# Performance work log

Hardware: AMD Instinct MI355X
Metric: run time of the kernel (lower is better)

## Reference

```python
import jax, jax.numpy as jnp
import numpy as np

B, N, DIN, DE, NH, DK = 4, 256, 128, 64, 8, 16


def setup_inputs() -> dict:
    key = jax.random.key(0)
    ks = jax.random.split(key, 8)
    s = 0.05
    return {
        "h": jax.random.normal(ks[0], (B, N, DIN), jnp.float32),
        "e": jax.random.normal(ks[1], (B, N, N, DE), jnp.float32),
        "mask": jnp.ones((B, N), jnp.float32),
        "WQ": jax.random.normal(ks[2], (DIN, NH * DK), jnp.float32) * s,
        "WK": jax.random.normal(ks[3], (DIN, NH * DK), jnp.float32) * s,
        "WV": jax.random.normal(ks[4], (DIN, NH * DK), jnp.float32) * s,
        "WE": jax.random.normal(ks[5], (DE, NH * DK), jnp.float32) * s,
        "WE2": jax.random.normal(ks[6], (DE, NH * DK), jnp.float32) * s,
    }


def reference(h, e, mask, WQ, WK, WV, WE, WE2):
    b, n, _ = h.shape
    Q = (h @ WQ).reshape(b, n, NH, DK)
    K = (h @ WK).reshape(b, n, NH, DK) * (float(DK) ** -0.5)
    V = (h @ WV).reshape(b, n, NH, DK)
    E = (e @ WE).reshape(b, n, n, NH, DK)
    E2 = (e @ WE2).reshape(b, n, n, NH, DK)
    # edge-augmented scores: (b, i, j, h, k)
    scores = jnp.einsum('bihk,bjhk->bijh', Q, K)[..., None] + E2
    scores = jnp.exp(jnp.clip(scores, -5.0, 5.0))
    attn_mask = mask[:, :, None, None, None] * mask[:, None, :, None, None]
    scores = scores * attn_mask
    softmax_denom = jnp.clip(scores.sum(axis=2), 1e-6, None)  # (b,i,h,k)
    scores = scores * attn_mask  # attn_dropout p=0.0 -> identity
    out = jnp.einsum('bijhk,bjhk->bihk', scores, V)
    out = out + (scores * E).sum(axis=2)
    out = out / softmax_denom
    return out.reshape(b, n, NH * DK)
```

## Files before the change

kernel.cpp:

```cpp
#include <hip/hip_runtime.h>

#define BB   4
#define NN   256
#define DIN  128
#define DE   64
#define NH   8
#define DK   16
#define CC   128

typedef __attribute__((ext_vector_type(8))) short short8;
typedef __attribute__((ext_vector_type(4))) float f32x4;

__device__ __forceinline__ unsigned short f2bfu(float f) {
    union { float f; unsigned int i; } v; v.f = f;
    unsigned int x = v.i;
    x += 0x7FFFu + ((x >> 16) & 1u);
    return (unsigned short)(x >> 16);
}

__global__ __launch_bounds__(256) void wprep_kernel(
    const float* __restrict__ WE, const float* __restrict__ WE2,
    unsigned short* __restrict__ wfrag)
{
    const int tid  = blockIdx.x * 256 + threadIdx.x;
    const int m    = tid >> 10;
    const int g    = (tid >> 7) & 7;
    const int ks   = (tid >> 6) & 1;
    const int lane = tid & 63;
    const int q4 = lane >> 4, l15 = lane & 15;
    const float* W = m ? WE2 : WE;
    union { uint4 u; unsigned short s[8]; } pk;
    #pragma unroll
    for (int ii = 0; ii < 8; ++ii) {
        const int d = ks * 32 + q4 * 8 + ii;
        pk.s[ii] = f2bfu(W[d * CC + g * 16 + l15]);
    }
    ((uint4*)wfrag)[tid] = pk.u;
}

__global__ __launch_bounds__(256) void qkv_kernel(
    const float* __restrict__ h, const float* __restrict__ WQ,
    const float* __restrict__ WK, const float* __restrict__ WV,
    float* __restrict__ Qw, float* __restrict__ Kw, float* __restrict__ Vw)
{
    __shared__ float hsh[4 * DIN];
    __shared__ float psum[4 * 1536];
    const int t  = threadIdx.x;
    const int r0 = blockIdx.x * 4;

    hsh[t]       = h[(size_t)r0 * DIN + t];
    hsh[256 + t] = h[(size_t)r0 * DIN + 256 + t];
    __syncthreads();

    const int cp  = t & 63;
    const int qtr = t >> 6;
    float aq[4][2], ak[4][2], av[4][2];
    #pragma unroll
    for (int r = 0; r < 4; ++r) {
        aq[r][0]=aq[r][1]=ak[r][0]=ak[r][1]=av[r][0]=av[r][1]=0.f;
    }
    #pragma unroll 4
    for (int dd = 0; dd < 32; ++dd) {
        const int d = qtr * 32 + dd;
        const float2 fq = ((const float2*)WQ)[d * 64 + cp];
        const float2 fk = ((const float2*)WK)[d * 64 + cp];
        const float2 fv = ((const float2*)WV)[d * 64 + cp];
        #pragma unroll
        for (int r = 0; r < 4; ++r) {
            const float hd = hsh[r * DIN + d];
            aq[r][0] = fmaf(hd, fq.x, aq[r][0]); aq[r][1] = fmaf(hd, fq.y, aq[r][1]);
            ak[r][0] = fmaf(hd, fk.x, ak[r][0]); ak[r][1] = fmaf(hd, fk.y, ak[r][1]);
            av[r][0] = fmaf(hd, fv.x, av[r][0]); av[r][1] = fmaf(hd, fv.y, av[r][1]);
        }
    }
    float* pq = psum + qtr * 1536;
    #pragma unroll
    for (int r = 0; r < 4; ++r) {
        pq[r*384       + 2*cp] = aq[r][0]; pq[r*384       + 2*cp+1] = aq[r][1];
        pq[r*384 + 128 + 2*cp] = ak[r][0]; pq[r*384 + 128 + 2*cp+1] = ak[r][1];
        pq[r*384 + 256 + 2*cp] = av[r][0]; pq[r*384 + 256 + 2*cp+1] = av[r][1];
    }
    __syncthreads();
    #pragma unroll
    for (int k = 0; k < 6; ++k) {
        const int o = k * 256 + t;
        float v = psum[o] + psum[1536 + o] + psum[3072 + o] + psum[4608 + o];
        const int r   = o / 384;
        const int mc  = o - r * 384;
        const int mat = mc >> 7;
        const int c   = mc & 127;
        const size_t idx = (size_t)(r0 + r) * CC + c;
        if      (mat == 0) Qw[idx] = v;
        else if (mat == 1) Kw[idx] = v * 0.25f;
        else               Vw[idx] = v;
    }
}

__global__ __launch_bounds__(256, 3) void attn_kernel(
    const float* __restrict__ e, const float* __restrict__ maskp,
    const unsigned short* __restrict__ wfrag,
    const float* __restrict__ Qw, const float* __restrict__ Kw,
    const float* __restrict__ Vw, float* __restrict__ out)
{
    __shared__ __align__(16) unsigned short esh[NN * DE];
    __shared__ float qk_sh[NN * 9];
    __shared__ float msk_sh[NN];
    __shared__ float qrow_sh[CC];

    const int row  = blockIdx.x;
    const int b    = row >> 8, i = row & 255;
    const int t    = threadIdx.x;
    const int wave = t >> 6, lane = t & 63;
    const int q4   = lane >> 4;
    const int l15  = lane & 15;

    {
        const float4* src = (const float4*)(e + (size_t)row * NN * DE);
        uint4* dst = (uint4*)esh;
        #pragma unroll
        for (int r = 0; r < 8; ++r) {
            const int cidx = r * 256 + t;
            const int j = cidx >> 3, ch = cidx & 7;
            const float4 f0 = src[2 * cidx];
            const float4 f1 = src[2 * cidx + 1];
            union { uint4 u; unsigned short s[8]; } pk;
            pk.s[0]=f2bfu(f0.x); pk.s[1]=f2bfu(f0.y); pk.s[2]=f2bfu(f0.z); pk.s[3]=f2bfu(f0.w);
            pk.s[4]=f2bfu(f1.x); pk.s[5]=f2bfu(f1.y); pk.s[6]=f2bfu(f1.z); pk.s[7]=f2bfu(f1.w);
            dst[j * 8 + (ch ^ (j & 7))] = pk.u;
        }
    }
    if (t < CC) qrow_sh[t] = Qw[(size_t)row * CC + t];
    msk_sh[t] = maskp[b * NN + t];

    short8 bfrag[2][2][2];
    {
        const uint4* wf = (const uint4*)wfrag;
        #pragma unroll
        for (int m = 0; m < 2; ++m)
        #pragma unroll
        for (int ct = 0; ct < 2; ++ct) {
            const int g = wave * 2 + ct;
            #pragma unroll
            for (int ks = 0; ks < 2; ++ks) {
                union { uint4 u; short8 s8; } cv;
                cv.u = wf[((m * 8 + g) * 2 + ks) * 64 + lane];
                bfrag[m][ct][ks] = cv.s8;
            }
        }
    }
    __syncthreads();

    {
        const float4* kr = (const float4*)(Kw + (size_t)(b * NN + t) * CC);
        #pragma unroll
        for (int hh = 0; hh < NH; ++hh) {
            float s = 0.f;
            #pragma unroll
            for (int p = 0; p < 4; ++p) {
                const float4 kv = kr[hh * 4 + p];
                const int qb = hh * 16 + p * 4;
                s += kv.x * qrow_sh[qb]     + kv.y * qrow_sh[qb + 1]
                   + kv.z * qrow_sh[qb + 2] + kv.w * qrow_sh[qb + 3];
            }
            qk_sh[t * 9 + hh] = s;
        }
    }
    __syncthreads();

    const float mi = msk_sh[i];
    float acc[2] = {0.f, 0.f}, dnm[2] = {0.f, 0.f};
    const short8* ep = (const short8*)esh;

    #pragma unroll 2
    for (int s = 0; s < 16; ++s) {
        const int ja = s * 16 + l15;
        const short8 a0 = ep[ja * 8 + ((q4    ) ^ (ja & 7))];
        const short8 a1 = ep[ja * 8 + ((q4 + 4) ^ (ja & 7))];
        #pragma unroll
        for (int ct = 0; ct < 2; ++ct) {
            const int g = wave * 2 + ct;
            f32x4 s2 = {0.f,0.f,0.f,0.f}, eE = {0.f,0.f,0.f,0.f};
            s2 = __builtin_amdgcn_mfma_f32_16x16x32_bf16(a0, bfrag[1][ct][0], s2, 0,0,0);
            s2 = __builtin_amdgcn_mfma_f32_16x16x32_bf16(a1, bfrag[1][ct][1], s2, 0,0,0);
            eE = __builtin_amdgcn_mfma_f32_16x16x32_bf16(a0, bfrag[0][ct][0], eE, 0,0,0);
            eE = __builtin_amdgcn_mfma_f32_16x16x32_bf16(a1, bfrag[0][ct][1], eE, 0,0,0);
            const float* vrow = Vw + (size_t)(b*NN + s*16 + q4*4) * CC + g*16 + l15;
            #pragma unroll
            for (int r = 0; r < 4; ++r) {
                const int jr = s * 16 + q4 * 4 + r;
                float sc = qk_sh[jr * 9 + g] + s2[r];
                sc = fminf(5.f, fmaxf(-5.f, sc));
                const float p  = __expf(sc);
                const float mm = mi * msk_sh[jr];
                const float s1 = p * mm;
                dnm[ct] += s1;
                const float vv = vrow[r * CC];
                acc[ct] = fmaf(s1 * mm, vv + eE[r], acc[ct]);
            }
        }
    }

    #pragma unroll
    for (int ct = 0; ct < 2; ++ct) {
        float a = acc[ct], d = dnm[ct];
        a += __shfl_xor(a, 16); a += __shfl_xor(a, 32);
        d += __shfl_xor(d, 16); d += __shfl_xor(d, 32);
        acc[ct] = a; dnm[ct] = d;
    }
    if (lane < 32) {
        const int ct = lane >> 4;
        out[(size_t)row * CC + wave * 32 + lane] = acc[ct] / fmaxf(dnm[ct], 1e-6f);
    }
}

extern "C" void kernel_launch(void* const* d_in, const int* in_sizes, int n_in,
                              void* d_out, int out_size, void* d_ws, size_t ws_size,
                              hipStream_t stream)
{
    const float* h    = (const float*)d_in[0];
    const float* e    = (const float*)d_in[1];
    const float* mask = (const float*)d_in[2];
    const float* WQ   = (const float*)d_in[3];
    const float* WK   = (const float*)d_in[4];
    const float* WV   = (const float*)d_in[5];
    const float* WE   = (const float*)d_in[6];
    const float* WE2  = (const float*)d_in[7];

    unsigned short* wfrag = (unsigned short*)d_ws;
    float* Qw = (float*)((char*)d_ws + 32768);
    float* Kw = Qw + BB * NN * CC;
    float* Vw = Kw + BB * NN * CC;

    wprep_kernel<<<8,   256, 0, stream>>>(WE, WE2, wfrag);
    qkv_kernel <<<256,  256, 0, stream>>>(h, WQ, WK, WV, Qw, Kw, Vw);
    attn_kernel<<<BB*NN, 256, 0, stream>>>(e, mask, wfrag, Qw, Kw, Vw,
                                           (float*)d_out);
}
```

Baseline: 139.9 us.

## Stream edge tiles through triple-buffered LDS and merge prep kernels

The attention kernel no longer stages the whole 256x64 edge row in LDS up front. It now loads 32-row tiles into registers one step ahead, converts them to bf16, and writes them into a 3-slot LDS ring, so global loads overlap with MFMA work. This shrinks LDS use and raises the occupancy hint from 3 to 4 blocks per CU. The weight-fragment prep and the QKV projection are also merged into a single launch to save one kernel launch. In exchange, the loop now has a barrier every tile and holds more registers for the prefetch.

```diff
diff --git a/kernel.cpp b/kernel.cpp
--- a/kernel.cpp
+++ b/kernel.cpp
@@ -18,36 +18,36 @@
     return (unsigned short)(x >> 16);
 }
 
-__global__ __launch_bounds__(256) void wprep_kernel(
-    const float* __restrict__ WE, const float* __restrict__ WE2,
-    unsigned short* __restrict__ wfrag)
-{
-    const int tid  = blockIdx.x * 256 + threadIdx.x;
-    const int m    = tid >> 10;
-    const int g    = (tid >> 7) & 7;
-    const int ks   = (tid >> 6) & 1;
-    const int lane = tid & 63;
-    const int q4 = lane >> 4, l15 = lane & 15;
-    const float* W = m ? WE2 : WE;
-    union { uint4 u; unsigned short s[8]; } pk;
-    #pragma unroll
-    for (int ii = 0; ii < 8; ++ii) {
-        const int d = ks * 32 + q4 * 8 + ii;
-        pk.s[ii] = f2bfu(W[d * CC + g * 16 + l15]);
-    }
-    ((uint4*)wfrag)[tid] = pk.u;
-}
-
-__global__ __launch_bounds__(256) void qkv_kernel(
+__global__ __launch_bounds__(256) void prep_kernel(
     const float* __restrict__ h, const float* __restrict__ WQ,
     const float* __restrict__ WK, const float* __restrict__ WV,
-    float* __restrict__ Qw, float* __restrict__ Kw, float* __restrict__ Vw)
+    const float* __restrict__ WE, const float* __restrict__ WE2,
+    float* __restrict__ Qw, float* __restrict__ Kw, float* __restrict__ Vw,
+    unsigned short* __restrict__ wfrag)
 {
     __shared__ float hsh[4 * DIN];
     __shared__ float psum[4 * 1536];
-    const int t  = threadIdx.x;
+    const int t = threadIdx.x;
+
+    if (blockIdx.x >= 256) {
+        const int tid  = (blockIdx.x - 256) * 256 + t;
+        const int m    = tid >> 10;
+        const int g    = (tid >> 7) & 7;
+        const int ks   = (tid >> 6) & 1;
+        const int lane = tid & 63;
+        const int q4 = lane >> 4, l15 = lane & 15;
+        const float* W = m ? WE2 : WE;
+        union { uint4 u; unsigned short s[8]; } pk;
+        #pragma unroll
+        for (int ii = 0; ii < 8; ++ii) {
+            const int d = ks * 32 + q4 * 8 + ii;
+            pk.s[ii] = f2bfu(W[d * CC + g * 16 + l15]);
+        }
+        ((uint4*)wfrag)[tid] = pk.u;
+        return;
+    }
+
     const int r0 = blockIdx.x * 4;
-
     hsh[t]       = h[(size_t)r0 * DIN + t];
     hsh[256 + t] = h[(size_t)r0 * DIN + 256 + t];
     __syncthreads();
@@ -96,13 +96,13 @@
     }
 }
 
-__global__ __launch_bounds__(256, 3) void attn_kernel(
+__global__ __launch_bounds__(256, 4) void attn_kernel(
     const float* __restrict__ e, const float* __restrict__ maskp,
     const unsigned short* __restrict__ wfrag,
     const float* __restrict__ Qw, const float* __restrict__ Kw,
     const float* __restrict__ Vw, float* __restrict__ out)
 {
-    __shared__ __align__(16) unsigned short esh[NN * DE];
+    __shared__ __align__(16) unsigned short esh[3][32 * DE];
     __shared__ float qk_sh[NN * 9];
     __shared__ float msk_sh[NN];
     __shared__ float qrow_sh[CC];
@@ -114,21 +114,16 @@
     const int q4   = lane >> 4;
     const int l15  = lane & 15;
 
-    {
-        const float4* src = (const float4*)(e + (size_t)row * NN * DE);
-        uint4* dst = (uint4*)esh;
-        #pragma unroll
-        for (int r = 0; r < 8; ++r) {
-            const int cidx = r * 256 + t;
-            const int j = cidx >> 3, ch = cidx & 7;
-            const float4 f0 = src[2 * cidx];
-            const float4 f1 = src[2 * cidx + 1];
-            union { uint4 u; unsigned short s[8]; } pk;
-            pk.s[0]=f2bfu(f0.x); pk.s[1]=f2bfu(f0.y); pk.s[2]=f2bfu(f0.z); pk.s[3]=f2bfu(f0.w);
-            pk.s[4]=f2bfu(f1.x); pk.s[5]=f2bfu(f1.y); pk.s[6]=f2bfu(f1.z); pk.s[7]=f2bfu(f1.w);
-            dst[j * 8 + (ch ^ (j & 7))] = pk.u;
-        }
-    }
+    const int sj_ = t >> 3;
+    const int sch = t & 7;
+    const float4* esrc = (const float4*)(e + (size_t)row * NN * DE)
+                         + (size_t)sj_ * 16 + sch * 2;
+    uint4* eshv = (uint4*)esh;
+
+    float4 pf[2][2];
+    pf[0][0] = esrc[0];       pf[0][1] = esrc[1];
+    pf[1][0] = esrc[512];     pf[1][1] = esrc[512 + 1];
+
     if (t < CC) qrow_sh[t] = Qw[(size_t)row * CC + t];
     msk_sh[t] = maskp[b * NN + t];
 
@@ -165,40 +160,61 @@
             qk_sh[t * 9 + hh] = s;
         }
     }
+
+#define STORE_TILE(BUF, F0, F1) {                                              \
+        union { uint4 u; unsigned short s[8]; } pk;                            \
+        pk.s[0]=f2bfu((F0).x); pk.s[1]=f2bfu((F0).y);                          \
+        pk.s[2]=f2bfu((F0).z); pk.s[3]=f2bfu((F0).w);                          \
+        pk.s[4]=f2bfu((F1).x); pk.s[5]=f2bfu((F1).y);                          \
+        pk.s[6]=f2bfu((F1).z); pk.s[7]=f2bfu((F1).w);                          \
+        eshv[(BUF)*256 + sj_*8 + (sch ^ (sj_ & 7))] = pk.u; }
+
+    STORE_TILE(0, pf[0][0], pf[0][1]);
     __syncthreads();
 
     const float mi = msk_sh[i];
     float acc[2] = {0.f, 0.f}, dnm[2] = {0.f, 0.f};
-    const short8* ep = (const short8*)esh;
-
-    #pragma unroll 2
-    for (int s = 0; s < 16; ++s) {
-        const int ja = s * 16 + l15;
-        const short8 a0 = ep[ja * 8 + ((q4    ) ^ (ja & 7))];
-        const short8 a1 = ep[ja * 8 + ((q4 + 4) ^ (ja & 7))];
-        #pragma unroll
-        for (int ct = 0; ct < 2; ++ct) {
-            const int g = wave * 2 + ct;
-            f32x4 s2 = {0.f,0.f,0.f,0.f}, eE = {0.f,0.f,0.f,0.f};
-            s2 = __builtin_amdgcn_mfma_f32_16x16x32_bf16(a0, bfrag[1][ct][0], s2, 0,0,0);
-            s2 = __builtin_amdgcn_mfma_f32_16x16x32_bf16(a1, bfrag[1][ct][1], s2, 0,0,0);
-            eE = __builtin_amdgcn_mfma_f32_16x16x32_bf16(a0, bfrag[0][ct][0], eE, 0,0,0);
-            eE = __builtin_amdgcn_mfma_f32_16x16x32_bf16(a1, bfrag[0][ct][1], eE, 0,0,0);
-            const float* vrow = Vw + (size_t)(b*NN + s*16 + q4*4) * CC + g*16 + l15;
+
+    #pragma unroll
+    for (int tt = 0; tt < 8; ++tt) {
+        if (tt < 6) {
+            pf[tt & 1][0] = esrc[(tt + 2) * 512];
+            pf[tt & 1][1] = esrc[(tt + 2) * 512 + 1];
+        }
+        const short8* ep = (const short8*)esh[tt % 3];
+        #pragma unroll
+        for (int sj = 0; sj < 2; ++sj) {
+            const int rloc = sj * 16 + l15;
+            const short8 a0 = ep[rloc * 8 + ((q4    ) ^ (rloc & 7))];
+            const short8 a1 = ep[rloc * 8 + ((q4 + 4) ^ (rloc & 7))];
+            const int jbase = tt * 32 + sj * 16;
             #pragma unroll
-            for (int r = 0; r < 4; ++r) {
-                const int jr = s * 16 + q4 * 4 + r;
-                float sc = qk_sh[jr * 9 + g] + s2[r];
-                sc = fminf(5.f, fmaxf(-5.f, sc));
-                const float p  = __expf(sc);
-                const float mm = mi * msk_sh[jr];
-                const float s1 = p * mm;
-                dnm[ct] += s1;
-                const float vv = vrow[r * CC];
-                acc[ct] = fmaf(s1 * mm, vv + eE[r], acc[ct]);
+            for (int ct = 0; ct < 2; ++ct) {
+                const int g = wave * 2 + ct;
+                f32x4 s2 = {0.f,0.f,0.f,0.f}, eE = {0.f,0.f,0.f,0.f};
+                s2 = __builtin_amdgcn_mfma_f32_16x16x32_bf16(a0, bfrag[1][ct][0], s2, 0,0,0);
+                s2 = __builtin_amdgcn_mfma_f32_16x16x32_bf16(a1, bfrag[1][ct][1], s2, 0,0,0);
+                eE = __builtin_amdgcn_mfma_f32_16x16x32_bf16(a0, bfrag[0][ct][0], eE, 0,0,0);
+                eE = __builtin_amdgcn_mfma_f32_16x16x32_bf16(a1, bfrag[0][ct][1], eE, 0,0,0);
+                const float* vrow = Vw + (size_t)(b*NN + jbase + q4*4) * CC + g*16 + l15;
+                #pragma unroll
+                for (int r = 0; r < 4; ++r) {
+                    const int jr = jbase + q4 * 4 + r;
+                    float sc = qk_sh[jr * 9 + g] + s2[r];
+                    sc = fminf(5.f, fmaxf(-5.f, sc));
+                    const float p  = __expf(sc);
+                    const float mm = mi * msk_sh[jr];
+                    const float s1 = p * mm;
+                    dnm[ct] += s1;
+                    const float vv = vrow[r * CC];
+                    acc[ct] = fmaf(s1 * mm, vv + eE[r], acc[ct]);
+                }
             }
         }
-    }
+        if (tt < 7) STORE_TILE((tt + 1) % 3, pf[(tt + 1) & 1][0], pf[(tt + 1) & 1][1]);
+        __syncthreads();
+    }
+#undef STORE_TILE
 
     #pragma unroll
     for (int ct = 0; ct < 2; ++ct) {
@@ -231,8 +247,8 @@
     float* Kw = Qw + BB * NN * CC;
     float* Vw = Kw + BB * NN * CC;
 
-    wprep_kernel<<<8,   256, 0, stream>>>(WE, WE2, wfrag);
-    qkv_kernel <<<256,  256, 0, stream>>>(h, WQ, WK, WV, Qw, Kw, Vw);
+    prep_kernel<<<264, 256, 0, stream>>>(h, WQ, WK, WV, WE, WE2,
+                                         Qw, Kw, Vw, wfrag);
     attn_kernel<<<BB*NN, 256, 0, stream>>>(e, mask, wfrag, Qw, Kw, Vw,
                                            (float*)d_out);
 }
```

After: 252.8 us. 1.81x slower.

## Merge prep kernels and widen attention blocks to 512 threads, one head per wave

Applied to the files above, without the earlier changes.

Folds the weight-fragment conversion into the QKV projection kernel as extra blocks, removing one launch. The attention kernel now runs 512 threads per row so each of 8 waves handles a single head instead of two, halving per-wave MFMA and softmax work. V loads and mask products are hoisted ahead of the MFMAs. The intent is more latency hiding per block and fewer serial steps per wave, at the cost of a larger block, with occupancy bounded by the 32KB of LDS each block holds for the e tile.

```diff
diff --git a/kernel.cpp b/kernel.cpp
--- a/kernel.cpp
+++ b/kernel.cpp
@@ -18,36 +18,36 @@
     return (unsigned short)(x >> 16);
 }
 
-__global__ __launch_bounds__(256) void wprep_kernel(
-    const float* __restrict__ WE, const float* __restrict__ WE2,
-    unsigned short* __restrict__ wfrag)
-{
-    const int tid  = blockIdx.x * 256 + threadIdx.x;
-    const int m    = tid >> 10;
-    const int g    = (tid >> 7) & 7;
-    const int ks   = (tid >> 6) & 1;
-    const int lane = tid & 63;
-    const int q4 = lane >> 4, l15 = lane & 15;
-    const float* W = m ? WE2 : WE;
-    union { uint4 u; unsigned short s[8]; } pk;
-    #pragma unroll
-    for (int ii = 0; ii < 8; ++ii) {
-        const int d = ks * 32 + q4 * 8 + ii;
-        pk.s[ii] = f2bfu(W[d * CC + g * 16 + l15]);
-    }
-    ((uint4*)wfrag)[tid] = pk.u;
-}
-
-__global__ __launch_bounds__(256) void qkv_kernel(
+__global__ __launch_bounds__(256) void prep_kernel(
     const float* __restrict__ h, const float* __restrict__ WQ,
     const float* __restrict__ WK, const float* __restrict__ WV,
-    float* __restrict__ Qw, float* __restrict__ Kw, float* __restrict__ Vw)
+    const float* __restrict__ WE, const float* __restrict__ WE2,
+    float* __restrict__ Qw, float* __restrict__ Kw, float* __restrict__ Vw,
+    unsigned short* __restrict__ wfrag)
 {
     __shared__ float hsh[4 * DIN];
     __shared__ float psum[4 * 1536];
-    const int t  = threadIdx.x;
+    const int t = threadIdx.x;
+
+    if (blockIdx.x >= 256) {
+        const int tid  = (blockIdx.x - 256) * 256 + t;
+        const int m    = tid >> 10;
+        const int g    = (tid >> 7) & 7;
+        const int ks   = (tid >> 6) & 1;
+        const int lane = tid & 63;
+        const int q4 = lane >> 4, l15 = lane & 15;
+        const float* W = m ? WE2 : WE;
+        union { uint4 u; unsigned short s[8]; } pk;
+        #pragma unroll
+        for (int ii = 0; ii < 8; ++ii) {
+            const int d = ks * 32 + q4 * 8 + ii;
+            pk.s[ii] = f2bfu(W[d * CC + g * 16 + l15]);
+        }
+        ((uint4*)wfrag)[tid] = pk.u;
+        return;
+    }
+
     const int r0 = blockIdx.x * 4;
-
     hsh[t]       = h[(size_t)r0 * DIN + t];
     hsh[256 + t] = h[(size_t)r0 * DIN + 256 + t];
     __syncthreads();
@@ -96,7 +96,7 @@
     }
 }
 
-__global__ __launch_bounds__(256, 3) void attn_kernel(
+__global__ __launch_bounds__(512, 6) void attn_kernel(
     const float* __restrict__ e, const float* __restrict__ maskp,
     const unsigned short* __restrict__ wfrag,
     const float* __restrict__ Qw, const float* __restrict__ Kw,
@@ -118,8 +118,8 @@
         const float4* src = (const float4*)(e + (size_t)row * NN * DE);
         uint4* dst = (uint4*)esh;
         #pragma unroll
-        for (int r = 0; r < 8; ++r) {
-            const int cidx = r * 256 + t;
+        for (int r = 0; r < 4; ++r) {
+            const int cidx = r * 512 + t;
             const int j = cidx >> 3, ch = cidx & 7;
             const float4 f0 = src[2 * cidx];
             const float4 f1 = src[2 * cidx + 1];
@@ -130,86 +130,87 @@
         }
     }
     if (t < CC) qrow_sh[t] = Qw[(size_t)row * CC + t];
-    msk_sh[t] = maskp[b * NN + t];
-
-    short8 bfrag[2][2][2];
+    if (t < NN) msk_sh[t] = maskp[b * NN + t];
+
+    short8 bfragE[2], bfragS[2];
     {
         const uint4* wf = (const uint4*)wfrag;
         #pragma unroll
-        for (int m = 0; m < 2; ++m)
-        #pragma unroll
-        for (int ct = 0; ct < 2; ++ct) {
-            const int g = wave * 2 + ct;
-            #pragma unroll
-            for (int ks = 0; ks < 2; ++ks) {
-                union { uint4 u; short8 s8; } cv;
-                cv.u = wf[((m * 8 + g) * 2 + ks) * 64 + lane];
-                bfrag[m][ct][ks] = cv.s8;
-            }
+        for (int ks = 0; ks < 2; ++ks) {
+            union { uint4 u; short8 s8; } cv;
+            cv.u = wf[((0 * 8 + wave) * 2 + ks) * 64 + lane];
+            bfragE[ks] = cv.s8;
+            cv.u = wf[((1 * 8 + wave) * 2 + ks) * 64 + lane];
+            bfragS[ks] = cv.s8;
         }
     }
     __syncthreads();
 
     {
-        const float4* kr = (const float4*)(Kw + (size_t)(b * NN + t) * CC);
-        #pragma unroll
-        for (int hh = 0; hh < NH; ++hh) {
+        const int j  = t & 255;
+        const int hb = (t >> 8) * 4;
+        const float4* kr = (const float4*)(Kw + (size_t)(b * NN + j) * CC);
+        #pragma unroll
+        for (int hh = 0; hh < 4; ++hh) {
+            const int hgl = hb + hh;
             float s = 0.f;
             #pragma unroll
             for (int p = 0; p < 4; ++p) {
-                const float4 kv = kr[hh * 4 + p];
-                const int qb = hh * 16 + p * 4;
+                const float4 kv = kr[hgl * 4 + p];
+                const int qb = hgl * 16 + p * 4;
                 s += kv.x * qrow_sh[qb]     + kv.y * qrow_sh[qb + 1]
                    + kv.z * qrow_sh[qb + 2] + kv.w * qrow_sh[qb + 3];
             }
-            qk_sh[t * 9 + hh] = s;
+            qk_sh[j * 9 + hgl] = s;
         }
     }
     __syncthreads();
 
     const float mi = msk_sh[i];
-    float acc[2] = {0.f, 0.f}, dnm[2] = {0.f, 0.f};
+    float acc = 0.f, dnm = 0.f;
     const short8* ep = (const short8*)esh;
+    const int g = wave;
 
     #pragma unroll 2
     for (int s = 0; s < 16; ++s) {
         const int ja = s * 16 + l15;
         const short8 a0 = ep[ja * 8 + ((q4    ) ^ (ja & 7))];
         const short8 a1 = ep[ja * 8 + ((q4 + 4) ^ (ja & 7))];
-        #pragma unroll
-        for (int ct = 0; ct < 2; ++ct) {
-            const int g = wave * 2 + ct;
-            f32x4 s2 = {0.f,0.f,0.f,0.f}, eE = {0.f,0.f,0.f,0.f};
-            s2 = __builtin_amdgcn_mfma_f32_16x16x32_bf16(a0, bfrag[1][ct][0], s2, 0,0,0);
-            s2 = __builtin_amdgcn_mfma_f32_16x16x32_bf16(a1, bfrag[1][ct][1], s2, 0,0,0);
-            eE = __builtin_amdgcn_mfma_f32_16x16x32_bf16(a0, bfrag[0][ct][0], eE, 0,0,0);
-            eE = __builtin_amdgcn_mfma_f32_16x16x32_bf16(a1, bfrag[0][ct][1], eE, 0,0,0);
+
+        float vv[4], qk[4], mm[4], mm2[4];
+        {
             const float* vrow = Vw + (size_t)(b*NN + s*16 + q4*4) * CC + g*16 + l15;
             #pragma unroll
-            for (int r = 0; r < 4; ++r) {
-                const int jr = s * 16 + q4 * 4 + r;
-                float sc = qk_sh[jr * 9 + g] + s2[r];
-                sc = fminf(5.f, fmaxf(-5.f, sc));
-                const float p  = __expf(sc);
-                const float mm = mi * msk_sh[jr];
-                const float s1 = p * mm;
-                dnm[ct] += s1;
-                const float vv = vrow[r * CC];
-                acc[ct] = fmaf(s1 * mm, vv + eE[r], acc[ct]);
-            }
-        }
-    }
-
-    #pragma unroll
-    for (int ct = 0; ct < 2; ++ct) {
-        float a = acc[ct], d = dnm[ct];
-        a += __shfl_xor(a, 16); a += __shfl_xor(a, 32);
-        d += __shfl_xor(d, 16); d += __shfl_xor(d, 32);
-        acc[ct] = a; dnm[ct] = d;
-    }
-    if (lane < 32) {
-        const int ct = lane >> 4;
-        out[(size_t)row * CC + wave * 32 + lane] = acc[ct] / fmaxf(dnm[ct], 1e-6f);
+            for (int r = 0; r < 4; ++r) vv[r] = vrow[r * CC];
+        }
+        #pragma unroll
+        for (int r = 0; r < 4; ++r) {
+            const int jr = s * 16 + q4 * 4 + r;
+            qk[r] = qk_sh[jr * 9 + g];
+            const float m = mi * msk_sh[jr];
+            mm[r] = m; mm2[r] = m * m;
+        }
+
+        f32x4 s2 = {0.f,0.f,0.f,0.f}, eE = {0.f,0.f,0.f,0.f};
+        s2 = __builtin_amdgcn_mfma_f32_16x16x32_bf16(a0, bfragS[0], s2, 0,0,0);
+        s2 = __builtin_amdgcn_mfma_f32_16x16x32_bf16(a1, bfragS[1], s2, 0,0,0);
+        eE = __builtin_amdgcn_mfma_f32_16x16x32_bf16(a0, bfragE[0], eE, 0,0,0);
+        eE = __builtin_amdgcn_mfma_f32_16x16x32_bf16(a1, bfragE[1], eE, 0,0,0);
+
+        #pragma unroll
+        for (int r = 0; r < 4; ++r) {
+            float sc = qk[r] + s2[r];
+            sc = fminf(5.f, fmaxf(-5.f, sc));
+            const float p = __expf(sc);
+            dnm += p * mm[r];
+            acc = fmaf(p * mm2[r], vv[r] + eE[r], acc);
+        }
+    }
+
+    acc += __shfl_xor(acc, 16); acc += __shfl_xor(acc, 32);
+    dnm += __shfl_xor(dnm, 16); dnm += __shfl_xor(dnm, 32);
+    if (lane < 16) {
+        out[(size_t)row * CC + g * 16 + lane] = acc / fmaxf(dnm, 1e-6f);
     }
 }
 
@@ -231,8 +232,8 @@
     float* Kw = Qw + BB * NN * CC;
     float* Vw = Kw + BB * NN * CC;
 
-    wprep_kernel<<<8,   256, 0, stream>>>(WE, WE2, wfrag);
-    qkv_kernel <<<256,  256, 0, stream>>>(h, WQ, WK, WV, Qw, Kw, Vw);
-    attn_kernel<<<BB*NN, 256, 0, stream>>>(e, mask, wfrag, Qw, Kw, Vw,
+    prep_kernel<<<264, 256, 0, stream>>>(h, WQ, WK, WV, WE, WE2,
+                                         Qw, Kw, Vw, wfrag);
+    attn_kernel<<<BB*NN, 512, 0, stream>>>(e, mask, wfrag, Qw, Kw, Vw,
                                            (float*)d_out);
 }
```

After: 138.7 us. No clear change (-0.9%).
